# Kernel optimization log

Measured on AMD Instinct MI355X. Metric: run time of the kernel, lower is better.

Reference implementation:

```python
import jax, jax.numpy as jnp
import numpy as np
from jax import lax

B, N, D = 4, 2048, 1024
MAX_SEQ = 2048
GROUPS = 4  # math.gcd(1024, 4)
LN_EPS = 1e-5


def setup_inputs() -> dict:
    key = jax.random.key(0)
    ks = jax.random.split(key, 12)
    s = 0.02
    return {
        "x": jax.random.normal(ks[0], (B, N, D), jnp.float32),
        "Wq": jax.random.normal(ks[1], (D, D), jnp.float32) * s,
        "Wk": jax.random.normal(ks[2], (D, D), jnp.float32) * s,
        "Wv": jax.random.normal(ks[3], (D, D), jnp.float32) * s,
        "rel_bias": jax.random.normal(ks[4], (1, MAX_SEQ, MAX_SEQ), jnp.float32) * s,
        "conv_w": jax.random.normal(ks[5], (D, D // GROUPS, 3), jnp.float32) * s,
        "conv_b": jnp.zeros((D,), jnp.float32),
        "resg_w": jax.random.normal(ks[6], (D, D), jnp.float32) * s,
        "resg_b": jnp.zeros((D,), jnp.float32),
        "ln_g": jnp.ones((D,), jnp.float32),
        "ln_b": jnp.zeros((D,), jnp.float32),
        "fc1_w": jax.random.normal(ks[7], (D // 2, D), jnp.float32) * s,
        "fc1_b": jnp.zeros((D // 2,), jnp.float32),
        "fc2_w": jax.random.normal(ks[8], (1, D // 2), jnp.float32) * s,
        "fc2_b": jnp.zeros((1,), jnp.float32),
    }


def _forward(x, Wq, Wk, Wv, rel_bias, conv_w, conv_b, resg_w, resg_b,
             ln_g, ln_b, fc1_w, fc1_b, fc2_w, fc2_b):
    b, n, d = x.shape
    scale = 1.0 / jnp.sqrt(jnp.asarray(d, x.dtype))
    q = x @ Wq.T  # [b,n,dk]
    k = x @ Wk.T
    v = x @ Wv.T  # [b,n,dv]
    att = jnp.einsum("bqd,bkd->bqk", q, k) * scale + rel_bias[:, :n, :n]
    causal = jnp.tril(jnp.ones((n, n), bool))
    att = jnp.where(causal, att, jnp.asarray(-jnp.inf, att.dtype))
    att = jax.nn.softmax(att, axis=-1)  # dropout is identity at eval
    att_out = jnp.einsum("bqk,bkd->bqd", att, v)
    # grouped temporal conv over sequence dim: v [b,n,dv] -> NCH [b,dv,n]
    conv = lax.conv_general_dilated(
        v.transpose(0, 2, 1), conv_w, window_strides=(1,), padding=[(1, 1)],
        dimension_numbers=("NCH", "OIH", "NCH"), feature_group_count=GROUPS)
    conv = conv + conv_b[None, :, None]
    out = att_out + conv.transpose(0, 2, 1)
    res = jax.nn.sigmoid(out @ resg_w.T + resg_b)
    out = x + res * out
    mu = out.mean(-1, keepdims=True)
    var = out.var(-1, keepdims=True)
    out = (out - mu) * lax.rsqrt(var + LN_EPS) * ln_g + ln_b
    h = jax.nn.gelu(out @ fc1_w.T + fc1_b, approximate=False)
    return jax.nn.sigmoid(h @ fc2_w.T + fc2_b)


def reference(x, Wq, Wk, Wv, rel_bias, conv_w, conv_b, resg_w, resg_b,
              ln_g, ln_b, fc1_w, fc1_b, fc2_w, fc2_b):
    return _forward(x, Wq, Wk, Wv, rel_bias, conv_w, conv_b, resg_w, resg_b,
                    ln_g, ln_b, fc1_w, fc1_b, fc2_w, fc2_b)
```

## Files before the change

kernel.cpp:

```cpp
#include <hip/hip_runtime.h>
#include <math.h>

#define NSEQ 2048
#define DDIM 1024
#define BSZ  4
#define BM 128
#define BN 128
#define BK 64

typedef short bf16x8 __attribute__((ext_vector_type(8)));
typedef float f32x4 __attribute__((ext_vector_type(4)));
typedef unsigned int u32;
typedef unsigned short u16;

__device__ __forceinline__ u16 f2bf(float f) {
  union { float f; u32 u; } x; x.f = f;
  u32 r = x.u + 0x7FFFu + ((x.u >> 16) & 1u);
  return (u16)(r >> 16);
}
__device__ __forceinline__ float bf2f(u16 h) {
  union { u32 u; float f; } x; x.u = ((u32)h) << 16; return x.f;
}
__device__ __forceinline__ float sigmoidf_(float x) {
  return 1.0f / (1.0f + expf(-x));
}

__device__ __forceinline__ void async_copy16(const u16* g, u16* l) {
  __builtin_amdgcn_global_load_lds(
      (const __attribute__((address_space(1))) u32*)g,
      (__attribute__((address_space(3))) u32*)l, 16, 0, 0);
}

__device__ __forceinline__ void stage_tile(const u16* __restrict__ gsrc, size_t ld,
                                           int k0, u16* lds, int tid) {
  const int wave = tid >> 6, lane = tid & 63;
  const int rr = lane >> 3;
  const int q  = (lane & 7) ^ rr;
#pragma unroll
  for (int j = 0; j < 4; ++j) {
    const int c = j * 4 + wave;
    async_copy16(gsrc + (size_t)(c * 8 + rr) * ld + k0 + q * 8, lds + c * 512);
  }
}

__device__ __forceinline__ void mfma_step(const u16* Al, const u16* Bl,
                                          int wr, int wc, int l16, int quad,
                                          f32x4 acc[4][4]) {
  const int r7 = l16 & 7;
#pragma unroll
  for (int ks = 0; ks < 2; ++ks) {
    const int s = ((ks * 4 + quad) ^ r7) << 3;
    bf16x8 a[4], b[4];
#pragma unroll
    for (int i = 0; i < 4; ++i) {
      a[i] = *(const bf16x8*)(Al + (wr * 64 + i * 16 + l16) * BK + s);
      b[i] = *(const bf16x8*)(Bl + (wc * 64 + i * 16 + l16) * BK + s);
    }
#pragma unroll
    for (int i = 0; i < 4; ++i)
#pragma unroll
      for (int j = 0; j < 4; ++j)
        acc[i][j] = __builtin_amdgcn_mfma_f32_16x16x32_bf16(a[i], b[j], acc[i][j], 0, 0, 0);
  }
}

__device__ __forceinline__ void zero_acc(f32x4 acc[4][4]) {
#pragma unroll
  for (int i = 0; i < 4; ++i)
#pragma unroll
    for (int j = 0; j < 4; ++j) {
      f32x4 z = {0.f, 0.f, 0.f, 0.f};
      acc[i][j] = z;
    }
}

__device__ __forceinline__ void gemm_loop(const u16* A, size_t lda,
                                          const u16* Bt, size_t ldb, int K,
                                          u16* Al, u16* Bl, int tid,
                                          int wr, int wc, int l16, int quad,
                                          f32x4 acc[4][4]) {
  for (int k0 = 0; k0 < K; k0 += BK) {
    __syncthreads();
    stage_tile(A, lda, k0, Al, tid);
    stage_tile(Bt, ldb, k0, Bl, tid);
    __syncthreads();
    mfma_step(Al, Bl, wr, wc, l16, quad, acc);
  }
}

__global__ __launch_bounds__(256) void k_prep(
    const float* __restrict__ x,  const float* __restrict__ Wq,
    const float* __restrict__ Wk, const float* __restrict__ Wv,
    const float* __restrict__ rw, const float* __restrict__ f1w,
    const float* __restrict__ cw,
    u16* __restrict__ xb,  u16* __restrict__ Wqb, u16* __restrict__ Wkb,
    u16* __restrict__ Wvb, u16* __restrict__ rwb, u16* __restrict__ f1wb,
    u16* __restrict__ cwp, u16* __restrict__ vpad)
{
  const int blk = blockIdx.x, tid = threadIdx.x;
  const float* s; u16* d; int base;
  if (blk < 8192)       { s = x;   d = xb;   base = blk; }
  else if (blk < 9216)  { s = Wq;  d = Wqb;  base = blk - 8192; }
  else if (blk < 10240) { s = Wk;  d = Wkb;  base = blk - 9216; }
  else if (blk < 11264) { s = Wv;  d = Wvb;  base = blk - 10240; }
  else if (blk < 12288) { s = rw;  d = rwb;  base = blk - 11264; }
  else if (blk < 12800) { s = f1w; d = f1wb; base = blk - 12288; }
  else if (blk < 13824) {
    const int o = blk - 12800, i = tid;
#pragma unroll
    for (int tap = 0; tap < 3; ++tap)
      cwp[(size_t)o * 768 + tap * 256 + i] = f2bf(cw[(size_t)o * 768 + i * 3 + tap]);
    return;
  } else {
    const int e = blk - 13824, bb = e >> 1, which = e & 1;
    u16* row = vpad + (size_t)bb * 2050 * 1024 + (which ? (size_t)2049 * 1024 : 0);
    ushort4 z = {0, 0, 0, 0};
    ((ushort4*)row)[tid] = z;
    return;
  }
  const int i = base * 256 + tid;
  const float4 v = ((const float4*)s)[i];
  ushort4 o;
  o.x = f2bf(v.x); o.y = f2bf(v.y); o.z = f2bf(v.z); o.w = f2bf(v.w);
  ((ushort4*)d)[i] = o;
}

__global__ __launch_bounds__(256) void k_qkv(
    const u16* __restrict__ xb, const u16* __restrict__ Wqb,
    const u16* __restrict__ Wkb, const u16* __restrict__ Wvb,
    u16* __restrict__ qb, u16* __restrict__ kb, u16* __restrict__ vpad)
{
  __shared__ u16 Al[BM * BK], Bl[BN * BK];
  const int tid = threadIdx.x, z = blockIdx.z;
  const u16* W = (z == 0) ? Wqb : ((z == 1) ? Wkb : Wvb);
  const int row0 = blockIdx.x * BM, col0 = blockIdx.y * BN;
  const int lane = tid & 63, wave = tid >> 6;
  const int quad = lane >> 4, l16 = lane & 15, wr = wave >> 1, wc = wave & 1;
  f32x4 acc[4][4];
  zero_acc(acc);
  gemm_loop(xb + (size_t)row0 * DDIM, DDIM, W + (size_t)col0 * DDIM, DDIM, DDIM,
            Al, Bl, tid, wr, wc, l16, quad, acc);
#pragma unroll
  for (int mi = 0; mi < 4; ++mi)
#pragma unroll
    for (int r = 0; r < 4; ++r) {
      const int grow = row0 + wr * 64 + mi * 16 + quad * 4 + r;
#pragma unroll
      for (int ni = 0; ni < 4; ++ni) {
        const int gcol = col0 + wc * 64 + ni * 16 + l16;
        const u16 hv = f2bf(acc[mi][ni][r]);
        if (z == 2) {
          const int b = grow >> 11, t = grow & 2047;
          vpad[(size_t)b * 2050 * 1024 + 1024 + (size_t)t * 1024 + gcol] = hv;
        } else {
          (z == 0 ? qb : kb)[(size_t)grow * DDIM + gcol] = hv;
        }
      }
    }
}

__global__ __launch_bounds__(256) void k_vt(const u16* __restrict__ vpad,
                                            u16* __restrict__ vT)
{
  __shared__ u16 tile[64][72];
  const int t0 = blockIdx.x * 64, d0 = blockIdx.y * 64, b = blockIdx.z;
  const int tid = threadIdx.x;
  const u16* vb = vpad + (size_t)b * 2050 * 1024 + 1024;
#pragma unroll
  for (int p = 0; p < 4; ++p) {
    const int r = p * 16 + (tid >> 4), c = (tid & 15) << 2;
    const ushort4 v4 = *(const ushort4*)(vb + (size_t)(t0 + r) * 1024 + d0 + c);
    tile[r][c] = v4.x; tile[r][c + 1] = v4.y; tile[r][c + 2] = v4.z; tile[r][c + 3] = v4.w;
  }
  __syncthreads();
  u16* ob = vT + (size_t)b * DDIM * NSEQ;
#pragma unroll
  for (int p = 0; p < 4; ++p) {
    const int d = p * 16 + (tid >> 4), t = (tid & 15) << 2;
    ushort4 o;
    o.x = tile[t][d]; o.y = tile[t + 1][d]; o.z = tile[t + 2][d]; o.w = tile[t + 3][d];
    *(ushort4*)(ob + (size_t)(d0 + d) * NSEQ + t0 + t) = o;
  }
}

__global__ __launch_bounds__(256) void k_scores(
    const u16* __restrict__ qb, const u16* __restrict__ kb,
    const float* __restrict__ rb, float* __restrict__ att)
{
  const int it = blockIdx.x, jt = blockIdx.y, b = blockIdx.z;
  if (jt > it) return;
  __shared__ u16 Al[BM * BK], Bl[BN * BK];
  const int tid = threadIdx.x;
  const int row0 = it * BM, col0 = jt * BN;
  const int lane = tid & 63, wave = tid >> 6;
  const int quad = lane >> 4, l16 = lane & 15, wr = wave >> 1, wc = wave & 1;
  f32x4 acc[4][4];
  zero_acc(acc);
  gemm_loop(qb + ((size_t)b * NSEQ + row0) * DDIM, DDIM,
            kb + ((size_t)b * NSEQ + col0) * DDIM, DDIM, DDIM,
            Al, Bl, tid, wr, wc, l16, quad, acc);
  float* abase = att + (size_t)b * NSEQ * NSEQ;
#pragma unroll
  for (int mi = 0; mi < 4; ++mi)
#pragma unroll
    for (int r = 0; r < 4; ++r) {
      const int i = row0 + wr * 64 + mi * 16 + quad * 4 + r;
#pragma unroll
      for (int ni = 0; ni < 4; ++ni) {
        const int j = col0 + wc * 64 + ni * 16 + l16;
        abase[(size_t)i * NSEQ + j] =
            acc[mi][ni][r] * 0.03125f + rb[(size_t)i * NSEQ + j];
      }
    }
}

__global__ __launch_bounds__(256) void k_softmax(const float* __restrict__ att,
                                                 u16* __restrict__ attb)
{
  const int i = blockIdx.x, b = blockIdx.y;
  const float* row = att + ((size_t)b * NSEQ + i) * NSEQ;
  u16* orow = attb + ((size_t)b * NSEQ + i) * NSEQ;
  const int valid = i + 1;
  const int wlen = ((i >> 7) + 1) << 7;
  const int tid = threadIdx.x;
  const int lane = tid & 63, wid = tid >> 6;

  float v[8];
  float m = -1e30f;
#pragma unroll
  for (int t = 0; t < 8; ++t) {
    const int idx = tid + (t << 8);
    v[t] = (idx < valid) ? row[idx] : -1e30f;
    m = fmaxf(m, v[t]);
  }
#pragma unroll
  for (int off = 32; off; off >>= 1) m = fmaxf(m, __shfl_xor(m, off));
  __shared__ float red[4];
  if (lane == 0) red[wid] = m;
  __syncthreads();
  m = fmaxf(fmaxf(red[0], red[1]), fmaxf(red[2], red[3]));
  __syncthreads();

  float s = 0.f;
#pragma unroll
  for (int t = 0; t < 8; ++t) {
    const int idx = tid + (t << 8);
    float e = (idx < valid) ? expf(v[t] - m) : 0.f;
    v[t] = e;
    s += e;
  }
#pragma unroll
  for (int off = 32; off; off >>= 1) s += __shfl_xor(s, off);
  if (lane == 0) red[wid] = s;
  __syncthreads();
  s = red[0] + red[1] + red[2] + red[3];
  const float inv = 1.0f / s;
#pragma unroll
  for (int t = 0; t < 8; ++t) {
    const int idx = tid + (t << 8);
    if (idx < wlen) orow[idx] = f2bf(v[t] * inv);
  }
}

__global__ __launch_bounds__(256) void k_pv(
    const u16* __restrict__ attb, const u16* __restrict__ vT,
    u16* __restrict__ pvb)
{
  __shared__ u16 Al[BM * BK], Bl[BN * BK];
  const int it = blockIdx.x, nt = blockIdx.y, b = blockIdx.z;
  const int tid = threadIdx.x;
  const int row0 = it * BM, col0 = nt * BN;
  const int K = (it + 1) * BM;
  const int lane = tid & 63, wave = tid >> 6;
  const int quad = lane >> 4, l16 = lane & 15, wr = wave >> 1, wc = wave & 1;
  f32x4 acc[4][4];
  zero_acc(acc);
  gemm_loop(attb + ((size_t)b * NSEQ + row0) * NSEQ, NSEQ,
            vT + ((size_t)b * DDIM + col0) * NSEQ, NSEQ, K,
            Al, Bl, tid, wr, wc, l16, quad, acc);
  u16* obase = pvb + (size_t)b * NSEQ * DDIM;
#pragma unroll
  for (int mi = 0; mi < 4; ++mi)
#pragma unroll
    for (int r = 0; r < 4; ++r) {
      const int grow = row0 + wr * 64 + mi * 16 + quad * 4 + r;
#pragma unroll
      for (int ni = 0; ni < 4; ++ni) {
        const int gcol = col0 + wc * 64 + ni * 16 + l16;
        obase[(size_t)grow * DDIM + gcol] = f2bf(acc[mi][ni][r]);
      }
    }
}

__global__ __launch_bounds__(256) void k_conv(
    const u16* __restrict__ vpad, const u16* __restrict__ cwp,
    const float* __restrict__ cb, const u16* __restrict__ pvb,
    u16* __restrict__ buf1b)
{
  __shared__ u16 Al[BM * BK], Bl[BN * BK];
  const int tid = threadIdx.x;
  const int row0 = blockIdx.x * BM;
  const int col0 = blockIdx.y * BN;
  const int g = col0 >> 8;
  const int b = row0 >> 11, t0 = row0 & 2047;
  const u16* vb = vpad + (size_t)b * 2050 * 1024 + 1024;
  const u16* Bbase = cwp + (size_t)col0 * 768;
  const int lane = tid & 63, wave = tid >> 6;
  const int quad = lane >> 4, l16 = lane & 15, wr = wave >> 1, wc = wave & 1;
  const int rr = lane >> 3;
  const int q  = (lane & 7) ^ rr;
  const int gch = g << 8;
  f32x4 acc[4][4];
  zero_acc(acc);
  for (int k0 = 0; k0 < 768; k0 += BK) {
    __syncthreads();
    const int tap = k0 >> 8;
    const int i0 = k0 & 255;
#pragma unroll
    for (int j = 0; j < 4; ++j) {
      const int c = j * 4 + wave;
      const int r = c * 8 + rr;
      async_copy16(vb + (size_t)(t0 + r - 1 + tap) * 1024 + gch + i0 + q * 8,
                   Al + c * 512);
    }
    stage_tile(Bbase, 768, k0, Bl, tid);
    __syncthreads();
    mfma_step(Al, Bl, wr, wc, l16, quad, acc);
  }
#pragma unroll
  for (int mi = 0; mi < 4; ++mi)
#pragma unroll
    for (int r = 0; r < 4; ++r) {
      const int grow = row0 + wr * 64 + mi * 16 + quad * 4 + r;
#pragma unroll
      for (int ni = 0; ni < 4; ++ni) {
        const int gcol = col0 + wc * 64 + ni * 16 + l16;
        const size_t idx = (size_t)grow * DDIM + gcol;
        buf1b[idx] = f2bf(bf2f(pvb[idx]) + cb[gcol] + acc[mi][ni][r]);
      }
    }
}

__global__ __launch_bounds__(256) void k_resgate(
    const u16* __restrict__ buf1b, const u16* __restrict__ rwb,
    const float* __restrict__ rbias, const float* __restrict__ x,
    u16* __restrict__ buf2)
{
  __shared__ u16 Al[BM * BK], Bl[BN * BK];
  const int tid = threadIdx.x;
  const int row0 = blockIdx.x * BM, col0 = blockIdx.y * BN;
  const int lane = tid & 63, wave = tid >> 6;
  const int quad = lane >> 4, l16 = lane & 15, wr = wave >> 1, wc = wave & 1;
  f32x4 acc[4][4];
  zero_acc(acc);
  gemm_loop(buf1b + (size_t)row0 * DDIM, DDIM, rwb + (size_t)col0 * DDIM, DDIM,
            DDIM, Al, Bl, tid, wr, wc, l16, quad, acc);
#pragma unroll
  for (int mi = 0; mi < 4; ++mi)
#pragma unroll
    for (int r = 0; r < 4; ++r) {
      const int grow = row0 + wr * 64 + mi * 16 + quad * 4 + r;
#pragma unroll
      for (int ni = 0; ni < 4; ++ni) {
        const int gcol = col0 + wc * 64 + ni * 16 + l16;
        const size_t idx = (size_t)grow * DDIM + gcol;
        const float gate = sigmoidf_(acc[mi][ni][r] + rbias[gcol]);
        buf2[idx] = f2bf(x[idx] + gate * bf2f(buf1b[idx]));
      }
    }
}

__global__ __launch_bounds__(256) void k_ln(
    const u16* __restrict__ buf, const float* __restrict__ gw,
    const float* __restrict__ gb, u16* __restrict__ outb)
{
  const int row = blockIdx.x;
  const u16* p = buf + (size_t)row * DDIM;
  const int tid = threadIdx.x;
  const int lane = tid & 63, wid = tid >> 6;
  const int c = tid << 2;
  const ushort4 raw = *(const ushort4*)(p + c);
  float4 val;
  val.x = bf2f(raw.x); val.y = bf2f(raw.y); val.z = bf2f(raw.z); val.w = bf2f(raw.w);
  float s = val.x + val.y + val.z + val.w;
  float s2 = val.x * val.x + val.y * val.y + val.z * val.z + val.w * val.w;
#pragma unroll
  for (int off = 32; off; off >>= 1) {
    s += __shfl_xor(s, off);
    s2 += __shfl_xor(s2, off);
  }
  __shared__ float r1[4], r2[4];
  if (lane == 0) { r1[wid] = s; r2[wid] = s2; }
  __syncthreads();
  s = r1[0] + r1[1] + r1[2] + r1[3];
  s2 = r2[0] + r2[1] + r2[2] + r2[3];
  const float mean = s * (1.0f / DDIM);
  const float var = s2 * (1.0f / DDIM) - mean * mean;
  const float rstd = rsqrtf(var + 1e-5f);
  const float4 g4 = *(const float4*)(gw + c);
  const float4 b4 = *(const float4*)(gb + c);
  ushort4 o;
  o.x = f2bf((val.x - mean) * rstd * g4.x + b4.x);
  o.y = f2bf((val.y - mean) * rstd * g4.y + b4.y);
  o.z = f2bf((val.z - mean) * rstd * g4.z + b4.z);
  o.w = f2bf((val.w - mean) * rstd * g4.w + b4.w);
  *(ushort4*)(outb + (size_t)row * DDIM + c) = o;
}

__global__ __launch_bounds__(256) void k_fc1(
    const u16* __restrict__ A, const u16* __restrict__ W,
    const float* __restrict__ bias, u16* __restrict__ h)
{
  __shared__ u16 Al[BM * BK], Bl[BN * BK];
  const int tid = threadIdx.x;
  const int row0 = blockIdx.x * BM, col0 = blockIdx.y * BN;
  const int lane = tid & 63, wave = tid >> 6;
  const int quad = lane >> 4, l16 = lane & 15, wr = wave >> 1, wc = wave & 1;
  f32x4 acc[4][4];
  zero_acc(acc);
  gemm_loop(A + (size_t)row0 * DDIM, DDIM, W + (size_t)col0 * DDIM, DDIM, DDIM,
            Al, Bl, tid, wr, wc, l16, quad, acc);
#pragma unroll
  for (int mi = 0; mi < 4; ++mi)
#pragma unroll
    for (int r = 0; r < 4; ++r) {
      const int grow = row0 + wr * 64 + mi * 16 + quad * 4 + r;
#pragma unroll
      for (int ni = 0; ni < 4; ++ni) {
        const int gcol = col0 + wc * 64 + ni * 16 + l16;
        const float t = acc[mi][ni][r] + bias[gcol];
        h[(size_t)grow * 512 + gcol] =
            f2bf(0.5f * t * (1.0f + erff(t * 0.70710678118654752f)));
      }
    }
}

__global__ __launch_bounds__(256) void k_fc2(
    const u16* __restrict__ h, const float* __restrict__ w,
    const float* __restrict__ b2, float* __restrict__ out)
{
  const int r = blockIdx.x * 4 + (threadIdx.x >> 6);
  const int lane = threadIdx.x & 63;
  const u16* hp = h + (size_t)r * 512;
  float s = 0.f;
#pragma unroll
  for (int t = 0; t < 8; ++t) {
    const int c = lane + t * 64;
    s = fmaf(bf2f(hp[c]), w[c], s);
  }
#pragma unroll
  for (int off = 32; off; off >>= 1) s += __shfl_xor(s, off);
  if (lane == 0) out[r] = sigmoidf_(s + b2[0]);
}

extern "C" void kernel_launch(void* const* d_in, const int* in_sizes, int n_in,
                              void* d_out, int out_size, void* d_ws, size_t ws_size,
                              hipStream_t stream) {
  const float* x    = (const float*)d_in[0];
  const float* Wq   = (const float*)d_in[1];
  const float* Wk   = (const float*)d_in[2];
  const float* Wv   = (const float*)d_in[3];
  const float* rb   = (const float*)d_in[4];
  const float* cw   = (const float*)d_in[5];
  const float* cb   = (const float*)d_in[6];
  const float* rw   = (const float*)d_in[7];
  const float* rbias= (const float*)d_in[8];
  const float* lng  = (const float*)d_in[9];
  const float* lnb  = (const float*)d_in[10];
  const float* f1w  = (const float*)d_in[11];
  const float* f1b  = (const float*)d_in[12];
  const float* f2w  = (const float*)d_in[13];
  const float* f2b  = (const float*)d_in[14];
  float* out = (float*)d_out;
  char* w8 = (char*)d_ws;

  u16* xb    = (u16*)(w8 + 0);
  u16* Wqb   = (u16*)(w8 + 16777216);
  u16* Wkb   = (u16*)(w8 + 18874368);
  u16* Wvb   = (u16*)(w8 + 20971520);
  u16* rwb   = (u16*)(w8 + 23068672);
  u16* f1wb  = (u16*)(w8 + 25165824);
  u16* cwp   = (u16*)(w8 + 26214400);
  u16* qb    = (u16*)(w8 + 27787264);
  u16* kb    = (u16*)(w8 + 44564480);
  u16* vpad  = (u16*)(w8 + 61341696);
  u16* vT    = (u16*)(w8 + 78135296);
  float* att = (float*)(w8 + 94912512);
  u16* attb  = (u16*)(w8 + 27787264);
  u16* pvb   = (u16*)(w8 + 94912512);
  u16* buf1b = (u16*)(w8 + 27787264);
  u16* buf2  = (u16*)(w8 + 111689728);
  u16* ln16  = (u16*)(w8 + 78135296);
  u16* h     = (u16*)(w8 + 61341696);

  k_prep   <<<dim3(13832),     256, 0, stream>>>(x, Wq, Wk, Wv, rw, f1w, cw,
                                                 xb, Wqb, Wkb, Wvb, rwb, f1wb,
                                                 cwp, vpad);
  k_qkv    <<<dim3(64, 8, 3),  256, 0, stream>>>(xb, Wqb, Wkb, Wvb, qb, kb, vpad);
  k_vt     <<<dim3(32, 16, 4), 256, 0, stream>>>(vpad, vT);
  k_scores <<<dim3(16, 16, 4), 256, 0, stream>>>(qb, kb, rb, att);
  k_softmax<<<dim3(NSEQ, BSZ), 256, 0, stream>>>(att, attb);
  k_pv     <<<dim3(16, 8, 4),  256, 0, stream>>>(attb, vT, pvb);
  k_conv   <<<dim3(64, 8),     256, 0, stream>>>(vpad, cwp, cb, pvb, buf1b);
  k_resgate<<<dim3(64, 8),     256, 0, stream>>>(buf1b, rwb, rbias, x, buf2);
  k_ln     <<<dim3(BSZ * NSEQ),256, 0, stream>>>(buf2, lng, lnb, ln16);
  k_fc1    <<<dim3(64, 4),     256, 0, stream>>>(ln16, f1wb, f1b, h);
  k_fc2    <<<dim3(NSEQ),      256, 0, stream>>>(h, f2w, f2b, out);
}
```

Baseline: 383.8 us.

## Merge scores, conv and V-transpose into one launch with packed causal score storage

Folds the causal score GEMM, the grouped conv GEMM and the V transpose into a single heterogeneous kernel with a flat grid. Only lower-triangular tiles are launched, and scores go to a packed triangular buffer instead of a full N×N array. The conv output now feeds the PV epilogue rather than the other way around, so the separate conv kernel and its re-read of PV are gone. rel_bias is converted to bf16 in the prep kernel, which halves bias reads in the score epilogue but adds a conversion pass and some bias precision loss.

```diff
diff --git a/kernel.cpp b/kernel.cpp
--- a/kernel.cpp
+++ b/kernel.cpp
@@ -88,14 +88,16 @@
   }
 }
 
+#define ATT_PB 2228224
+
 __global__ __launch_bounds__(256) void k_prep(
     const float* __restrict__ x,  const float* __restrict__ Wq,
     const float* __restrict__ Wk, const float* __restrict__ Wv,
     const float* __restrict__ rw, const float* __restrict__ f1w,
-    const float* __restrict__ cw,
+    const float* __restrict__ rb, const float* __restrict__ cw,
     u16* __restrict__ xb,  u16* __restrict__ Wqb, u16* __restrict__ Wkb,
     u16* __restrict__ Wvb, u16* __restrict__ rwb, u16* __restrict__ f1wb,
-    u16* __restrict__ cwp, u16* __restrict__ vpad)
+    u16* __restrict__ rbb, u16* __restrict__ cwp, u16* __restrict__ vpad)
 {
   const int blk = blockIdx.x, tid = threadIdx.x;
   const float* s; u16* d; int base;
@@ -105,14 +107,15 @@
   else if (blk < 11264) { s = Wv;  d = Wvb;  base = blk - 10240; }
   else if (blk < 12288) { s = rw;  d = rwb;  base = blk - 11264; }
   else if (blk < 12800) { s = f1w; d = f1wb; base = blk - 12288; }
-  else if (blk < 13824) {
-    const int o = blk - 12800, i = tid;
+  else if (blk < 16896) { s = rb;  d = rbb;  base = blk - 12800; }
+  else if (blk < 17920) {
+    const int o = blk - 16896, i = tid;
 #pragma unroll
     for (int tap = 0; tap < 3; ++tap)
       cwp[(size_t)o * 768 + tap * 256 + i] = f2bf(cw[(size_t)o * 768 + i * 3 + tap]);
     return;
   } else {
-    const int e = blk - 13824, bb = e >> 1, which = e & 1;
+    const int e = blk - 17920, bb = e >> 1, which = e & 1;
     u16* row = vpad + (size_t)bb * 2050 * 1024 + (which ? (size_t)2049 * 1024 : 0);
     ushort4 z = {0, 0, 0, 0};
     ((ushort4*)row)[tid] = z;
@@ -159,69 +162,122 @@
     }
 }
 
-__global__ __launch_bounds__(256) void k_vt(const u16* __restrict__ vpad,
-                                            u16* __restrict__ vT)
-{
-  __shared__ u16 tile[64][72];
-  const int t0 = blockIdx.x * 64, d0 = blockIdx.y * 64, b = blockIdx.z;
-  const int tid = threadIdx.x;
-  const u16* vb = vpad + (size_t)b * 2050 * 1024 + 1024;
-#pragma unroll
-  for (int p = 0; p < 4; ++p) {
-    const int r = p * 16 + (tid >> 4), c = (tid & 15) << 2;
-    const ushort4 v4 = *(const ushort4*)(vb + (size_t)(t0 + r) * 1024 + d0 + c);
-    tile[r][c] = v4.x; tile[r][c + 1] = v4.y; tile[r][c + 2] = v4.z; tile[r][c + 3] = v4.w;
-  }
-  __syncthreads();
-  u16* ob = vT + (size_t)b * DDIM * NSEQ;
-#pragma unroll
-  for (int p = 0; p < 4; ++p) {
-    const int d = p * 16 + (tid >> 4), t = (tid & 15) << 2;
-    ushort4 o;
-    o.x = tile[t][d]; o.y = tile[t + 1][d]; o.z = tile[t + 2][d]; o.w = tile[t + 3][d];
-    *(ushort4*)(ob + (size_t)(d0 + d) * NSEQ + t0 + t) = o;
-  }
-}
-
-__global__ __launch_bounds__(256) void k_scores(
+__global__ __launch_bounds__(256) void k_phaseA(
     const u16* __restrict__ qb, const u16* __restrict__ kb,
-    const float* __restrict__ rb, float* __restrict__ att)
-{
-  const int it = blockIdx.x, jt = blockIdx.y, b = blockIdx.z;
-  if (jt > it) return;
-  __shared__ u16 Al[BM * BK], Bl[BN * BK];
-  const int tid = threadIdx.x;
-  const int row0 = it * BM, col0 = jt * BN;
+    const u16* __restrict__ rbb, float* __restrict__ attp,
+    const u16* __restrict__ vpad, const u16* __restrict__ cwp,
+    const float* __restrict__ cb, u16* __restrict__ convb,
+    u16* __restrict__ vT)
+{
+  __shared__ __align__(16) u16 SM[BM * BK + BN * BK];
+  u16* Al = SM;
+  u16* Bl = SM + BM * BK;
+  const int id = blockIdx.x, tid = threadIdx.x;
   const int lane = tid & 63, wave = tid >> 6;
   const int quad = lane >> 4, l16 = lane & 15, wr = wave >> 1, wc = wave & 1;
-  f32x4 acc[4][4];
-  zero_acc(acc);
-  gemm_loop(qb + ((size_t)b * NSEQ + row0) * DDIM, DDIM,
-            kb + ((size_t)b * NSEQ + col0) * DDIM, DDIM, DDIM,
-            Al, Bl, tid, wr, wc, l16, quad, acc);
-  float* abase = att + (size_t)b * NSEQ * NSEQ;
-#pragma unroll
-  for (int mi = 0; mi < 4; ++mi)
-#pragma unroll
-    for (int r = 0; r < 4; ++r) {
-      const int i = row0 + wr * 64 + mi * 16 + quad * 4 + r;
-#pragma unroll
-      for (int ni = 0; ni < 4; ++ni) {
-        const int j = col0 + wc * 64 + ni * 16 + l16;
-        abase[(size_t)i * NSEQ + j] =
-            acc[mi][ni][r] * 0.03125f + rb[(size_t)i * NSEQ + j];
-      }
-    }
-}
-
-__global__ __launch_bounds__(256) void k_softmax(const float* __restrict__ att,
+
+  if (id < 544) {
+    const int b = id / 136, t = id - b * 136;
+    int it = (int)((sqrtf(8.f * t + 1.f) - 1.f) * 0.5f);
+    while ((it + 1) * (it + 2) / 2 <= t) ++it;
+    while (it * (it + 1) / 2 > t) --it;
+    const int jt = t - it * (it + 1) / 2;
+    const int row0 = it * BM, col0 = jt * BN;
+    f32x4 acc[4][4];
+    zero_acc(acc);
+    gemm_loop(qb + ((size_t)b * NSEQ + row0) * DDIM, DDIM,
+              kb + ((size_t)b * NSEQ + col0) * DDIM, DDIM, DDIM,
+              Al, Bl, tid, wr, wc, l16, quad, acc);
+    float* abase = attp + (size_t)b * ATT_PB + (size_t)(it * (it + 1) / 2) * 16384;
+    const int ldp = (it + 1) * 128;
+#pragma unroll
+    for (int mi = 0; mi < 4; ++mi)
+#pragma unroll
+      for (int r = 0; r < 4; ++r) {
+        const int ri = wr * 64 + mi * 16 + quad * 4 + r;
+        const int gi = row0 + ri;
+#pragma unroll
+        for (int ni = 0; ni < 4; ++ni) {
+          const int j = col0 + wc * 64 + ni * 16 + l16;
+          abase[(size_t)ri * ldp + j] =
+              acc[mi][ni][r] * 0.03125f + bf2f(rbb[(size_t)gi * NSEQ + j]);
+        }
+      }
+  } else if (id < 1056) {
+    const int id2 = id - 544;
+    const int row0 = (id2 >> 3) * BM;
+    const int col0 = (id2 & 7) * BN;
+    const int g = col0 >> 8;
+    const int b = row0 >> 11, t0 = row0 & 2047;
+    const u16* vb = vpad + (size_t)b * 2050 * 1024 + 1024;
+    const u16* Bbase = cwp + (size_t)col0 * 768;
+    const int rr = lane >> 3;
+    const int q  = (lane & 7) ^ rr;
+    const int gch = g << 8;
+    f32x4 acc[4][4];
+    zero_acc(acc);
+    for (int k0 = 0; k0 < 768; k0 += BK) {
+      __syncthreads();
+      const int tap = k0 >> 8;
+      const int i0 = k0 & 255;
+#pragma unroll
+      for (int j = 0; j < 4; ++j) {
+        const int c = j * 4 + wave;
+        const int r = c * 8 + rr;
+        async_copy16(vb + (size_t)(t0 + r - 1 + tap) * 1024 + gch + i0 + q * 8,
+                     Al + c * 512);
+      }
+      stage_tile(Bbase, 768, k0, Bl, tid);
+      __syncthreads();
+      mfma_step(Al, Bl, wr, wc, l16, quad, acc);
+    }
+#pragma unroll
+    for (int mi = 0; mi < 4; ++mi)
+#pragma unroll
+      for (int r = 0; r < 4; ++r) {
+        const int grow = row0 + wr * 64 + mi * 16 + quad * 4 + r;
+#pragma unroll
+        for (int ni = 0; ni < 4; ++ni) {
+          const int gcol = col0 + wc * 64 + ni * 16 + l16;
+          convb[(size_t)grow * DDIM + gcol] = f2bf(cb[gcol] + acc[mi][ni][r]);
+        }
+      }
+  } else {
+    const int id3 = id - 1056;
+    const int b = id3 >> 9, rem = id3 & 511;
+    const int t0 = (rem & 31) * 64, d0 = (rem >> 5) * 64;
+    u16* tile = SM;
+    const u16* vb = vpad + (size_t)b * 2050 * 1024 + 1024;
+#pragma unroll
+    for (int p = 0; p < 4; ++p) {
+      const int r = p * 16 + (tid >> 4), c = (tid & 15) << 2;
+      const ushort4 v4 = *(const ushort4*)(vb + (size_t)(t0 + r) * 1024 + d0 + c);
+      tile[r * 72 + c] = v4.x; tile[r * 72 + c + 1] = v4.y;
+      tile[r * 72 + c + 2] = v4.z; tile[r * 72 + c + 3] = v4.w;
+    }
+    __syncthreads();
+    u16* ob = vT + (size_t)b * DDIM * NSEQ;
+#pragma unroll
+    for (int p = 0; p < 4; ++p) {
+      const int d = p * 16 + (tid >> 4), tt = (tid & 15) << 2;
+      ushort4 o;
+      o.x = tile[tt * 72 + d]; o.y = tile[(tt + 1) * 72 + d];
+      o.z = tile[(tt + 2) * 72 + d]; o.w = tile[(tt + 3) * 72 + d];
+      *(ushort4*)(ob + (size_t)(d0 + d) * NSEQ + t0 + tt) = o;
+    }
+  }
+}
+
+__global__ __launch_bounds__(256) void k_softmax(const float* __restrict__ attp,
                                                  u16* __restrict__ attb)
 {
   const int i = blockIdx.x, b = blockIdx.y;
-  const float* row = att + ((size_t)b * NSEQ + i) * NSEQ;
+  const int it = i >> 7;
+  const int wlen = (it + 1) << 7;
+  const float* row = attp + (size_t)b * ATT_PB +
+                     (size_t)(it * (it + 1) / 2) * 16384 + (size_t)(i & 127) * wlen;
   u16* orow = attb + ((size_t)b * NSEQ + i) * NSEQ;
   const int valid = i + 1;
-  const int wlen = ((i >> 7) + 1) << 7;
   const int tid = threadIdx.x;
   const int lane = tid & 63, wid = tid >> 6;
 
@@ -264,7 +320,7 @@
 
 __global__ __launch_bounds__(256) void k_pv(
     const u16* __restrict__ attb, const u16* __restrict__ vT,
-    u16* __restrict__ pvb)
+    const u16* __restrict__ convb, u16* __restrict__ buf1b)
 {
   __shared__ u16 Al[BM * BK], Bl[BN * BK];
   const int it = blockIdx.x, nt = blockIdx.y, b = blockIdx.z;
@@ -278,7 +334,7 @@
   gemm_loop(attb + ((size_t)b * NSEQ + row0) * NSEQ, NSEQ,
             vT + ((size_t)b * DDIM + col0) * NSEQ, NSEQ, K,
             Al, Bl, tid, wr, wc, l16, quad, acc);
-  u16* obase = pvb + (size_t)b * NSEQ * DDIM;
+  const size_t obase = (size_t)b * NSEQ * DDIM;
 #pragma unroll
   for (int mi = 0; mi < 4; ++mi)
 #pragma unroll
@@ -287,56 +343,8 @@
 #pragma unroll
       for (int ni = 0; ni < 4; ++ni) {
         const int gcol = col0 + wc * 64 + ni * 16 + l16;
-        obase[(size_t)grow * DDIM + gcol] = f2bf(acc[mi][ni][r]);
-      }
-    }
-}
-
-__global__ __launch_bounds__(256) void k_conv(
-    const u16* __restrict__ vpad, const u16* __restrict__ cwp,
-    const float* __restrict__ cb, const u16* __restrict__ pvb,
-    u16* __restrict__ buf1b)
-{
-  __shared__ u16 Al[BM * BK], Bl[BN * BK];
-  const int tid = threadIdx.x;
-  const int row0 = blockIdx.x * BM;
-  const int col0 = blockIdx.y * BN;
-  const int g = col0 >> 8;
-  const int b = row0 >> 11, t0 = row0 & 2047;
-  const u16* vb = vpad + (size_t)b * 2050 * 1024 + 1024;
-  const u16* Bbase = cwp + (size_t)col0 * 768;
-  const int lane = tid & 63, wave = tid >> 6;
-  const int quad = lane >> 4, l16 = lane & 15, wr = wave >> 1, wc = wave & 1;
-  const int rr = lane >> 3;
-  const int q  = (lane & 7) ^ rr;
-  const int gch = g << 8;
-  f32x4 acc[4][4];
-  zero_acc(acc);
-  for (int k0 = 0; k0 < 768; k0 += BK) {
-    __syncthreads();
-    const int tap = k0 >> 8;
-    const int i0 = k0 & 255;
-#pragma unroll
-    for (int j = 0; j < 4; ++j) {
-      const int c = j * 4 + wave;
-      const int r = c * 8 + rr;
-      async_copy16(vb + (size_t)(t0 + r - 1 + tap) * 1024 + gch + i0 + q * 8,
-                   Al + c * 512);
-    }
-    stage_tile(Bbase, 768, k0, Bl, tid);
-    __syncthreads();
-    mfma_step(Al, Bl, wr, wc, l16, quad, acc);
-  }
-#pragma unroll
-  for (int mi = 0; mi < 4; ++mi)
-#pragma unroll
-    for (int r = 0; r < 4; ++r) {
-      const int grow = row0 + wr * 64 + mi * 16 + quad * 4 + r;
-#pragma unroll
-      for (int ni = 0; ni < 4; ++ni) {
-        const int gcol = col0 + wc * 64 + ni * 16 + l16;
-        const size_t idx = (size_t)grow * DDIM + gcol;
-        buf1b[idx] = f2bf(bf2f(pvb[idx]) + cb[gcol] + acc[mi][ni][r]);
+        const size_t idx = obase + (size_t)grow * DDIM + gcol;
+        buf1b[idx] = f2bf(acc[mi][ni][r] + bf2f(convb[idx]));
       }
     }
 }
@@ -485,23 +493,23 @@
   u16* kb    = (u16*)(w8 + 44564480);
   u16* vpad  = (u16*)(w8 + 61341696);
   u16* vT    = (u16*)(w8 + 78135296);
-  float* att = (float*)(w8 + 94912512);
+  float* attp= (float*)(w8 + 94912512);
+  u16* convb = (u16*)(w8 + 130564096);
+  u16* rbb   = (u16*)(w8 + 147341312);
   u16* attb  = (u16*)(w8 + 27787264);
-  u16* pvb   = (u16*)(w8 + 94912512);
-  u16* buf1b = (u16*)(w8 + 27787264);
-  u16* buf2  = (u16*)(w8 + 111689728);
+  u16* buf1b = (u16*)(w8 + 0);
+  u16* buf2  = (u16*)(w8 + 27787264);
   u16* ln16  = (u16*)(w8 + 78135296);
   u16* h     = (u16*)(w8 + 61341696);
 
-  k_prep   <<<dim3(13832),     256, 0, stream>>>(x, Wq, Wk, Wv, rw, f1w, cw,
+  k_prep   <<<dim3(17928),     256, 0, stream>>>(x, Wq, Wk, Wv, rw, f1w, rb, cw,
                                                  xb, Wqb, Wkb, Wvb, rwb, f1wb,
-                                                 cwp, vpad);
+                                                 rbb, cwp, vpad);
   k_qkv    <<<dim3(64, 8, 3),  256, 0, stream>>>(xb, Wqb, Wkb, Wvb, qb, kb, vpad);
-  k_vt     <<<dim3(32, 16, 4), 256, 0, stream>>>(vpad, vT);
-  k_scores <<<dim3(16, 16, 4), 256, 0, stream>>>(qb, kb, rb, att);
-  k_softmax<<<dim3(NSEQ, BSZ), 256, 0, stream>>>(att, attb);
-  k_pv     <<<dim3(16, 8, 4),  256, 0, stream>>>(attb, vT, pvb);
-  k_conv   <<<dim3(64, 8),     256, 0, stream>>>(vpad, cwp, cb, pvb, buf1b);
+  k_phaseA <<<dim3(3104),      256, 0, stream>>>(qb, kb, rbb, attp, vpad, cwp,
+                                                 cb, convb, vT);
+  k_softmax<<<dim3(NSEQ, BSZ), 256, 0, stream>>>(attp, attb);
+  k_pv     <<<dim3(16, 8, 4),  256, 0, stream>>>(attb, vT, convb, buf1b);
   k_resgate<<<dim3(64, 8),     256, 0, stream>>>(buf1b, rwb, rbias, x, buf2);
   k_ln     <<<dim3(BSZ * NSEQ),256, 0, stream>>>(buf2, lng, lnb, ln16);
   k_fc1    <<<dim3(64, 4),     256, 0, stream>>>(ln16, f1wb, f1b, h);
```

New measurement: 389.3 us. No clear change (+1.4%).

## Pack causal score tiles, launch only lower-triangle blocks, fuse conv into PV epilogue

Applied to the files above, without the earlier changes.

Scores are now stored in a packed lower-triangular layout, and only the 136 causal tiles per batch are launched instead of 256 blocks with early exits. Softmax reads the matching packed rows. The conv kernel now runs before attention and writes its output with bias, and the PV kernel adds that in its epilogue, removing the separate read of the PV result. Workspace buffers are rearranged to fit the new layout, and each score block pays a small loop to map its index to a tile.

```diff
diff --git a/kernel.cpp b/kernel.cpp
--- a/kernel.cpp
+++ b/kernel.cpp
@@ -88,6 +88,8 @@
   }
 }
 
+#define ATT_PB 2228224
+
 __global__ __launch_bounds__(256) void k_prep(
     const float* __restrict__ x,  const float* __restrict__ Wq,
     const float* __restrict__ Wk, const float* __restrict__ Wv,
@@ -183,119 +185,9 @@
   }
 }
 
-__global__ __launch_bounds__(256) void k_scores(
-    const u16* __restrict__ qb, const u16* __restrict__ kb,
-    const float* __restrict__ rb, float* __restrict__ att)
-{
-  const int it = blockIdx.x, jt = blockIdx.y, b = blockIdx.z;
-  if (jt > it) return;
-  __shared__ u16 Al[BM * BK], Bl[BN * BK];
-  const int tid = threadIdx.x;
-  const int row0 = it * BM, col0 = jt * BN;
-  const int lane = tid & 63, wave = tid >> 6;
-  const int quad = lane >> 4, l16 = lane & 15, wr = wave >> 1, wc = wave & 1;
-  f32x4 acc[4][4];
-  zero_acc(acc);
-  gemm_loop(qb + ((size_t)b * NSEQ + row0) * DDIM, DDIM,
-            kb + ((size_t)b * NSEQ + col0) * DDIM, DDIM, DDIM,
-            Al, Bl, tid, wr, wc, l16, quad, acc);
-  float* abase = att + (size_t)b * NSEQ * NSEQ;
-#pragma unroll
-  for (int mi = 0; mi < 4; ++mi)
-#pragma unroll
-    for (int r = 0; r < 4; ++r) {
-      const int i = row0 + wr * 64 + mi * 16 + quad * 4 + r;
-#pragma unroll
-      for (int ni = 0; ni < 4; ++ni) {
-        const int j = col0 + wc * 64 + ni * 16 + l16;
-        abase[(size_t)i * NSEQ + j] =
-            acc[mi][ni][r] * 0.03125f + rb[(size_t)i * NSEQ + j];
-      }
-    }
-}
-
-__global__ __launch_bounds__(256) void k_softmax(const float* __restrict__ att,
-                                                 u16* __restrict__ attb)
-{
-  const int i = blockIdx.x, b = blockIdx.y;
-  const float* row = att + ((size_t)b * NSEQ + i) * NSEQ;
-  u16* orow = attb + ((size_t)b * NSEQ + i) * NSEQ;
-  const int valid = i + 1;
-  const int wlen = ((i >> 7) + 1) << 7;
-  const int tid = threadIdx.x;
-  const int lane = tid & 63, wid = tid >> 6;
-
-  float v[8];
-  float m = -1e30f;
-#pragma unroll
-  for (int t = 0; t < 8; ++t) {
-    const int idx = tid + (t << 8);
-    v[t] = (idx < valid) ? row[idx] : -1e30f;
-    m = fmaxf(m, v[t]);
-  }
-#pragma unroll
-  for (int off = 32; off; off >>= 1) m = fmaxf(m, __shfl_xor(m, off));
-  __shared__ float red[4];
-  if (lane == 0) red[wid] = m;
-  __syncthreads();
-  m = fmaxf(fmaxf(red[0], red[1]), fmaxf(red[2], red[3]));
-  __syncthreads();
-
-  float s = 0.f;
-#pragma unroll
-  for (int t = 0; t < 8; ++t) {
-    const int idx = tid + (t << 8);
-    float e = (idx < valid) ? expf(v[t] - m) : 0.f;
-    v[t] = e;
-    s += e;
-  }
-#pragma unroll
-  for (int off = 32; off; off >>= 1) s += __shfl_xor(s, off);
-  if (lane == 0) red[wid] = s;
-  __syncthreads();
-  s = red[0] + red[1] + red[2] + red[3];
-  const float inv = 1.0f / s;
-#pragma unroll
-  for (int t = 0; t < 8; ++t) {
-    const int idx = tid + (t << 8);
-    if (idx < wlen) orow[idx] = f2bf(v[t] * inv);
-  }
-}
-
-__global__ __launch_bounds__(256) void k_pv(
-    const u16* __restrict__ attb, const u16* __restrict__ vT,
-    u16* __restrict__ pvb)
-{
-  __shared__ u16 Al[BM * BK], Bl[BN * BK];
-  const int it = blockIdx.x, nt = blockIdx.y, b = blockIdx.z;
-  const int tid = threadIdx.x;
-  const int row0 = it * BM, col0 = nt * BN;
-  const int K = (it + 1) * BM;
-  const int lane = tid & 63, wave = tid >> 6;
-  const int quad = lane >> 4, l16 = lane & 15, wr = wave >> 1, wc = wave & 1;
-  f32x4 acc[4][4];
-  zero_acc(acc);
-  gemm_loop(attb + ((size_t)b * NSEQ + row0) * NSEQ, NSEQ,
-            vT + ((size_t)b * DDIM + col0) * NSEQ, NSEQ, K,
-            Al, Bl, tid, wr, wc, l16, quad, acc);
-  u16* obase = pvb + (size_t)b * NSEQ * DDIM;
-#pragma unroll
-  for (int mi = 0; mi < 4; ++mi)
-#pragma unroll
-    for (int r = 0; r < 4; ++r) {
-      const int grow = row0 + wr * 64 + mi * 16 + quad * 4 + r;
-#pragma unroll
-      for (int ni = 0; ni < 4; ++ni) {
-        const int gcol = col0 + wc * 64 + ni * 16 + l16;
-        obase[(size_t)grow * DDIM + gcol] = f2bf(acc[mi][ni][r]);
-      }
-    }
-}
-
 __global__ __launch_bounds__(256) void k_conv(
     const u16* __restrict__ vpad, const u16* __restrict__ cwp,
-    const float* __restrict__ cb, const u16* __restrict__ pvb,
-    u16* __restrict__ buf1b)
+    const float* __restrict__ cb, u16* __restrict__ convb)
 {
   __shared__ u16 Al[BM * BK], Bl[BN * BK];
   const int tid = threadIdx.x;
@@ -335,8 +227,122 @@
 #pragma unroll
       for (int ni = 0; ni < 4; ++ni) {
         const int gcol = col0 + wc * 64 + ni * 16 + l16;
-        const size_t idx = (size_t)grow * DDIM + gcol;
-        buf1b[idx] = f2bf(bf2f(pvb[idx]) + cb[gcol] + acc[mi][ni][r]);
+        convb[(size_t)grow * DDIM + gcol] = f2bf(cb[gcol] + acc[mi][ni][r]);
+      }
+    }
+}
+
+__global__ __launch_bounds__(256) void k_scores(
+    const u16* __restrict__ qb, const u16* __restrict__ kb,
+    const float* __restrict__ rb, float* __restrict__ attp)
+{
+  __shared__ u16 Al[BM * BK], Bl[BN * BK];
+  const int b = blockIdx.x, t = blockIdx.y, tid = threadIdx.x;
+  int it = 0;
+  while ((it + 1) * (it + 2) / 2 <= t) ++it;
+  const int jt = t - it * (it + 1) / 2;
+  const int row0 = it * BM, col0 = jt * BN;
+  const int lane = tid & 63, wave = tid >> 6;
+  const int quad = lane >> 4, l16 = lane & 15, wr = wave >> 1, wc = wave & 1;
+  f32x4 acc[4][4];
+  zero_acc(acc);
+  gemm_loop(qb + ((size_t)b * NSEQ + row0) * DDIM, DDIM,
+            kb + ((size_t)b * NSEQ + col0) * DDIM, DDIM, DDIM,
+            Al, Bl, tid, wr, wc, l16, quad, acc);
+  float* abase = attp + (size_t)b * ATT_PB + (size_t)(it * (it + 1) / 2) * 16384;
+  const int ldp = (it + 1) * 128;
+#pragma unroll
+  for (int mi = 0; mi < 4; ++mi)
+#pragma unroll
+    for (int r = 0; r < 4; ++r) {
+      const int ri = wr * 64 + mi * 16 + quad * 4 + r;
+      const int gi = row0 + ri;
+#pragma unroll
+      for (int ni = 0; ni < 4; ++ni) {
+        const int j = col0 + wc * 64 + ni * 16 + l16;
+        abase[(size_t)ri * ldp + j] =
+            acc[mi][ni][r] * 0.03125f + rb[(size_t)gi * NSEQ + j];
+      }
+    }
+}
+
+__global__ __launch_bounds__(256) void k_softmax(const float* __restrict__ attp,
+                                                 u16* __restrict__ attb)
+{
+  const int i = blockIdx.x, b = blockIdx.y;
+  const int it = i >> 7;
+  const int wlen = (it + 1) << 7;
+  const float* row = attp + (size_t)b * ATT_PB +
+                     (size_t)(it * (it + 1) / 2) * 16384 + (size_t)(i & 127) * wlen;
+  u16* orow = attb + ((size_t)b * NSEQ + i) * NSEQ;
+  const int valid = i + 1;
+  const int tid = threadIdx.x;
+  const int lane = tid & 63, wid = tid >> 6;
+
+  float v[8];
+  float m = -1e30f;
+#pragma unroll
+  for (int t = 0; t < 8; ++t) {
+    const int idx = tid + (t << 8);
+    v[t] = (idx < valid) ? row[idx] : -1e30f;
+    m = fmaxf(m, v[t]);
+  }
+#pragma unroll
+  for (int off = 32; off; off >>= 1) m = fmaxf(m, __shfl_xor(m, off));
+  __shared__ float red[4];
+  if (lane == 0) red[wid] = m;
+  __syncthreads();
+  m = fmaxf(fmaxf(red[0], red[1]), fmaxf(red[2], red[3]));
+  __syncthreads();
+
+  float s = 0.f;
+#pragma unroll
+  for (int t = 0; t < 8; ++t) {
+    const int idx = tid + (t << 8);
+    float e = (idx < valid) ? expf(v[t] - m) : 0.f;
+    v[t] = e;
+    s += e;
+  }
+#pragma unroll
+  for (int off = 32; off; off >>= 1) s += __shfl_xor(s, off);
+  if (lane == 0) red[wid] = s;
+  __syncthreads();
+  s = red[0] + red[1] + red[2] + red[3];
+  const float inv = 1.0f / s;
+#pragma unroll
+  for (int t = 0; t < 8; ++t) {
+    const int idx = tid + (t << 8);
+    if (idx < wlen) orow[idx] = f2bf(v[t] * inv);
+  }
+}
+
+__global__ __launch_bounds__(256) void k_pv(
+    const u16* __restrict__ attb, const u16* __restrict__ vT,
+    const u16* __restrict__ convb, u16* __restrict__ buf1b)
+{
+  __shared__ u16 Al[BM * BK], Bl[BN * BK];
+  const int it = blockIdx.x, nt = blockIdx.y, b = blockIdx.z;
+  const int tid = threadIdx.x;
+  const int row0 = it * BM, col0 = nt * BN;
+  const int K = (it + 1) * BM;
+  const int lane = tid & 63, wave = tid >> 6;
+  const int quad = lane >> 4, l16 = lane & 15, wr = wave >> 1, wc = wave & 1;
+  f32x4 acc[4][4];
+  zero_acc(acc);
+  gemm_loop(attb + ((size_t)b * NSEQ + row0) * NSEQ, NSEQ,
+            vT + ((size_t)b * DDIM + col0) * NSEQ, NSEQ, K,
+            Al, Bl, tid, wr, wc, l16, quad, acc);
+  const size_t obase = (size_t)b * NSEQ * DDIM;
+#pragma unroll
+  for (int mi = 0; mi < 4; ++mi)
+#pragma unroll
+    for (int r = 0; r < 4; ++r) {
+      const int grow = row0 + wr * 64 + mi * 16 + quad * 4 + r;
+#pragma unroll
+      for (int ni = 0; ni < 4; ++ni) {
+        const int gcol = col0 + wc * 64 + ni * 16 + l16;
+        const size_t idx = obase + (size_t)grow * DDIM + gcol;
+        buf1b[idx] = f2bf(acc[mi][ni][r] + bf2f(convb[idx]));
       }
     }
 }
@@ -485,11 +491,11 @@
   u16* kb    = (u16*)(w8 + 44564480);
   u16* vpad  = (u16*)(w8 + 61341696);
   u16* vT    = (u16*)(w8 + 78135296);
-  float* att = (float*)(w8 + 94912512);
+  float* attp= (float*)(w8 + 94912512);
+  u16* convb = (u16*)(w8 + 130564096);
   u16* attb  = (u16*)(w8 + 27787264);
-  u16* pvb   = (u16*)(w8 + 94912512);
-  u16* buf1b = (u16*)(w8 + 27787264);
-  u16* buf2  = (u16*)(w8 + 111689728);
+  u16* buf1b = (u16*)(w8 + 0);
+  u16* buf2  = (u16*)(w8 + 27787264);
   u16* ln16  = (u16*)(w8 + 78135296);
   u16* h     = (u16*)(w8 + 61341696);
 
@@ -498,10 +504,10 @@
                                                  cwp, vpad);
   k_qkv    <<<dim3(64, 8, 3),  256, 0, stream>>>(xb, Wqb, Wkb, Wvb, qb, kb, vpad);
   k_vt     <<<dim3(32, 16, 4), 256, 0, stream>>>(vpad, vT);
-  k_scores <<<dim3(16, 16, 4), 256, 0, stream>>>(qb, kb, rb, att);
-  k_softmax<<<dim3(NSEQ, BSZ), 256, 0, stream>>>(att, attb);
-  k_pv     <<<dim3(16, 8, 4),  256, 0, stream>>>(attb, vT, pvb);
-  k_conv   <<<dim3(64, 8),     256, 0, stream>>>(vpad, cwp, cb, pvb, buf1b);
+  k_conv   <<<dim3(64, 8),     256, 0, stream>>>(vpad, cwp, cb, convb);
+  k_scores <<<dim3(4, 136),    256, 0, stream>>>(qb, kb, rb, attp);
+  k_softmax<<<dim3(NSEQ, BSZ), 256, 0, stream>>>(attp, attb);
+  k_pv     <<<dim3(16, 8, 4),  256, 0, stream>>>(attb, vT, convb, buf1b);
   k_resgate<<<dim3(64, 8),     256, 0, stream>>>(buf1b, rwb, rbias, x, buf2);
   k_ln     <<<dim3(BSZ * NSEQ),256, 0, stream>>>(buf2, lng, lnb, ln16);
   k_fc1    <<<dim3(64, 4),     256, 0, stream>>>(ln16, f1wb, f1b, h);
```

New measurement: 380.4 us. About the same (-0.9%).
